# Optimization experiments

Hardware: AMD Instinct MI355X
Metric: run time of the kernel (lower is better)

Reference implementation:

```python
import jax, jax.numpy as jnp
import numpy as np

HEAD_DIM = 64
N_IT = 3
EPS = 1.0  # SinkhornDistance(1, max_iter=n_it)
SCALE = 1.0 / float(np.sqrt(HEAD_DIM))


def setup_inputs() -> dict:
    key = jax.random.key(0)
    kq, kk, kv = jax.random.split(key, 3)
    B, H, S, D = 2, 12, 1024, HEAD_DIM
    q = jax.random.normal(kq, (B, H, S, D), dtype=jnp.float32)
    k = jax.random.normal(kk, (B, H, S, D), dtype=jnp.float32)
    v = jax.random.normal(kv, (B, H, S, D), dtype=jnp.float32)
    attn_mask = jnp.zeros((1, 1, S, S), dtype=bool)  # False -> no position masked
    return {"q": q, "k": k, "v": v, "attn_mask": attn_mask}


def _sinkhorn(scores):
    # Log-domain Sinkhorn-Knopp (sinkformers-style). Cost C = -scores,
    # uniform marginals mu = nu = 1/S, u/v initialized to zero.
    C = -scores                                   # [N, S, S]
    n = C.shape[-2]
    m = C.shape[-1]
    log_mu = -jnp.log(jnp.asarray(n, C.dtype))    # log(1/n)
    log_nu = -jnp.log(jnp.asarray(m, C.dtype))    # log(1/m)

    def M(u, v):
        # modified cost matrix: (-C + u_i + v_j) / eps
        return (-C + u[..., :, None] + v[..., None, :]) / EPS

    def body(carry, _):
        u, v = carry
        u = EPS * (log_mu - jax.scipy.special.logsumexp(M(u, v), axis=-1)) + u
        v = EPS * (log_nu - jax.scipy.special.logsumexp(M(u, v), axis=-2)) + v
        return (u, v), None

    u0 = jnp.zeros(C.shape[:-1], C.dtype)
    v0 = jnp.zeros(C.shape[:-2] + (m,), C.dtype)
    (u, v), _ = jax.lax.scan(body, (u0, v0), None, length=N_IT)
    return jnp.exp(M(u, v))                       # transport plan pi, rows/cols ~ 1/S


def reference(q, k, v, attn_mask):
    B, H, S, D = q.shape
    scores = jnp.einsum('bhqd,bhkd->bhqk', q, k) * SCALE
    scores = jnp.where(attn_mask, jnp.asarray(-1e9, scores.dtype), scores)
    pi = _sinkhorn(scores.reshape(B * H, S, S))
    # pi rows sum to ~1/S; multiply by S so rows sum to ~1 (as in the torch code)
    attn_weights = (pi * S).reshape(B, H, S, S)
    output = jnp.einsum('bhqk,bhkd->bhqd', attn_weights, v)
    return output, attn_weights
```

## Files before the change

### kernel.cpp

```cpp
#include <hip/hip_runtime.h>
#include <hip/hip_fp16.h>
#include <cstddef>
#include <cstdint>


#define NH 24
#define SEQ 1024
#define HD 64
#define NHS (NH * SEQ)

typedef _Float16 f16x8 __attribute__((ext_vector_type(8)));
typedef float f32x4 __attribute__((ext_vector_type(4)));

__global__ __launch_bounds__(256) void k_prep(const float* __restrict__ q,
                                              const float* __restrict__ kin,
                                              const float* __restrict__ v,
                                              __half* __restrict__ q16,
                                              __half* __restrict__ k16,
                                              __half* __restrict__ vt16,
                                              float* __restrict__ zvec) {
  const int b = blockIdx.x;
  const int z = b / 768;
  const int bb = b - z * 768;
  const int t = threadIdx.x;
  if (z < 2) {
    const float* src = z ? kin : q;
    __half* dst = z ? k16 : q16;
    size_t u = ((size_t)bb * 256 + t) * 8;
    const float4* s4 = (const float4*)(src + u);
    float4 a = s4[0], c = s4[1];
    f16x8 h;
    h[0] = (_Float16)a.x; h[1] = (_Float16)a.y; h[2] = (_Float16)a.z; h[3] = (_Float16)a.w;
    h[4] = (_Float16)c.x; h[5] = (_Float16)c.y; h[6] = (_Float16)c.z; h[7] = (_Float16)c.w;
    *(f16x8*)(dst + u) = h;
    if (z == 0) {
      int gid = bb * 256 + t;
      if (gid < 6 * NHS) zvec[gid] = 0.f;
    }
  } else {
    __shared__ float ld[64][33];
    const int h = bb >> 5, s0 = (bb & 31) << 5;
    const float* Vh = v + (size_t)h * SEQ * HD;
#pragma unroll
    for (int it = 0; it < 2; ++it) {
      int f = t + (it << 8);
      int r = f >> 4, c4 = (f & 15) << 2;
      float4 vv = *(const float4*)(Vh + (size_t)(s0 + r) * HD + c4);
      ld[c4 + 0][r] = vv.x; ld[c4 + 1][r] = vv.y;
      ld[c4 + 2][r] = vv.z; ld[c4 + 3][r] = vv.w;
    }
    __syncthreads();
    int d = t >> 2, sg = (t & 3) << 3;
    f16x8 h8;
#pragma unroll
    for (int i = 0; i < 8; ++i) h8[i] = (_Float16)ld[d][sg + i];
    *(f16x8*)(vt16 + (size_t)h * HD * SEQ + (size_t)d * SEQ + s0 + sg) = h8;
  }
}

template <int MODE>
__global__ __launch_bounds__(256) void k_sweep(const __half* __restrict__ q16,
                                               const __half* __restrict__ k16,
                                               const float* __restrict__ vecPrev,
                                               float* __restrict__ vecOut) {
  __shared__ __align__(16) __half ks[128][72];
  __shared__ float ws_[128];
  const int bid = blockIdx.x;
  const int swz = (bid & 7) * 192 + (bid >> 3);
  const int h = swz >> 6;
  const int row0 = ((swz >> 3) & 7) << 7;
  const int col0 = (swz & 7) << 7;
  const int t = threadIdx.x;
  const int w = t >> 6, lane = t & 63;
  const int ln = lane & 15, ko = lane >> 4;
  const int rb = (w & 1) << 6, cb = (w >> 1) << 6;
  const __half* qh = q16 + ((size_t)h << 16);
  const __half* kh = k16 + ((size_t)h << 16);

#pragma unroll
  for (int it = 0; it < 4; ++it) {
    int f = t + (it << 8);
    int row = f >> 3, c8 = (f & 7) << 3;
    *(f16x8*)&ks[row][c8] = *(const f16x8*)(kh + (size_t)(col0 + row) * HD + c8);
  }
  if (MODE == 1 && t < 128) ws_[t] = (1.0f / 1024.0f) / vecPrev[h * SEQ + col0 + t];
  if (MODE == 2 && t < 128) ws_[t] = (1.0f / 1024.0f) / vecPrev[h * SEQ + row0 + t];
  f16x8 af[4][2];
#pragma unroll
  for (int m = 0; m < 4; ++m)
#pragma unroll
    for (int kk = 0; kk < 2; ++kk)
      af[m][kk] = *(const f16x8*)(qh + (size_t)(row0 + rb + m * 16 + ln) * HD + kk * 32 + ko * 8);
  __syncthreads();

  f32x4 acc[4][4] = {};
#pragma unroll
  for (int kk = 0; kk < 2; ++kk) {
    f16x8 bf[4];
#pragma unroll
    for (int n = 0; n < 4; ++n)
      bf[n] = *(const f16x8*)&ks[cb + n * 16 + ln][kk * 32 + ko * 8];
#pragma unroll
    for (int m = 0; m < 4; ++m)
#pragma unroll
      for (int n = 0; n < 4; ++n)
        acc[m][n] = __builtin_amdgcn_mfma_f32_16x16x32_f16(af[m][kk], bf[n], acc[m][n], 0, 0, 0);
  }

#pragma unroll
  for (int m = 0; m < 4; ++m)
#pragma unroll
    for (int n = 0; n < 4; ++n)
#pragma unroll
      for (int r = 0; r < 4; ++r)
        acc[m][n][r] = __expf(acc[m][n][r] * 0.125f);

  if (MODE == 2) {
    float* cs = vecOut + h * SEQ;
#pragma unroll
    for (int n = 0; n < 4; ++n) {
      float s = 0.f;
#pragma unroll
      for (int m = 0; m < 4; ++m)
#pragma unroll
        for (int r = 0; r < 4; ++r)
          s += acc[m][n][r] * ws_[rb + m * 16 + (ko << 2) + r];
      s += __shfl_xor(s, 16);
      s += __shfl_xor(s, 32);
      if (lane < 16) atomicAdd(&cs[col0 + cb + n * 16 + ln], s);
    }
  } else {
    float* rd = vecOut + h * SEQ;
#pragma unroll
    for (int m = 0; m < 4; ++m)
#pragma unroll
      for (int r = 0; r < 4; ++r) {
        float s;
        if (MODE == 1) {
          s = acc[m][0][r] * ws_[cb + ln] + acc[m][1][r] * ws_[cb + 16 + ln]
            + acc[m][2][r] * ws_[cb + 32 + ln] + acc[m][3][r] * ws_[cb + 48 + ln];
        } else {
          s = acc[m][0][r] + acc[m][1][r] + acc[m][2][r] + acc[m][3][r];
        }
        s += __shfl_xor(s, 1, 16); s += __shfl_xor(s, 2, 16);
        s += __shfl_xor(s, 4, 16); s += __shfl_xor(s, 8, 16);
        if (ln == 0) atomicAdd(&rd[row0 + rb + m * 16 + (ko << 2) + r], s);
      }
  }
}

__global__ __launch_bounds__(256) void k_final(const __half* __restrict__ q16,
                                               const __half* __restrict__ k16,
                                               const __half* __restrict__ vt16,
                                               const float* __restrict__ rd2,
                                               const float* __restrict__ cs2,
                                               float* __restrict__ attn,
                                               float* __restrict__ out) {
  __shared__ __align__(16) __half ps16[2][16][136];
  __shared__ float binv[1024];
  __shared__ float a_s[16];
  const int bid = blockIdx.x;
  const int swz = (bid & 7) * 192 + (bid >> 3);
  const int h = swz >> 6;
  const int rblk = swz & 63;
  const int t = threadIdx.x;
  const int w = t >> 6, lane = t & 63, ln = lane & 15, ko = lane >> 4;

#pragma unroll
  for (int i = 0; i < 4; ++i) {
    int idx = t + (i << 8);
    binv[idx] = 1.0f / cs2[h * SEQ + idx];
  }
  if (t < 16) a_s[t] = (1.0f / 1024.0f) / rd2[h * SEQ + rblk * 16 + t];

  const __half* qh = q16 + ((size_t)h << 16);
  const __half* kh = k16 + ((size_t)h << 16);
  const __half* vth = vt16 + ((size_t)h << 16);
  f16x8 aq[2];
#pragma unroll
  for (int kk = 0; kk < 2; ++kk)
    aq[kk] = *(const f16x8*)(qh + (size_t)(rblk * 16 + ln) * HD + kk * 32 + ko * 8);

  const int cw = w << 5;
  const int dw = w << 4;

  f16x8 kf00, kf01, kf10, kf11;
  kf00 = *(const f16x8*)(kh + (size_t)(cw + ln) * HD + ko * 8);
  kf01 = *(const f16x8*)(kh + (size_t)(cw + 16 + ln) * HD + ko * 8);
  kf10 = *(const f16x8*)(kh + (size_t)(cw + ln) * HD + 32 + ko * 8);
  kf11 = *(const f16x8*)(kh + (size_t)(cw + 16 + ln) * HD + 32 + ko * 8);
  f16x8 vf0, vf1, vf2, vf3;
  {
    const __half* vb = vth + (size_t)(dw + ln) * SEQ;
    vf0 = *(const f16x8*)(vb + ko * 8);
    vf1 = *(const f16x8*)(vb + 32 + ko * 8);
    vf2 = *(const f16x8*)(vb + 64 + ko * 8);
    vf3 = *(const f16x8*)(vb + 96 + ko * 8);
  }
  f32x4 sacc0 = {}, sacc1 = {};
  sacc0 = __builtin_amdgcn_mfma_f32_16x16x32_f16(aq[0], kf00, sacc0, 0, 0, 0);
  sacc1 = __builtin_amdgcn_mfma_f32_16x16x32_f16(aq[0], kf01, sacc1, 0, 0, 0);
  sacc0 = __builtin_amdgcn_mfma_f32_16x16x32_f16(aq[1], kf10, sacc0, 0, 0, 0);
  sacc1 = __builtin_amdgcn_mfma_f32_16x16x32_f16(aq[1], kf11, sacc1, 0, 0, 0);
  f32x4 acc_o = {};
  __syncthreads();

  for (int c = 0; c < 8; ++c) {
    const int j0 = c << 7;
    const int buf = c & 1;
    f16x8 kn00, kn01, kn10, kn11, vn0, vn1, vn2, vn3;
    if (c < 7) {
      const __half* kb = kh + (size_t)(j0 + 128) * HD;
      kn00 = *(const f16x8*)(kb + (size_t)(cw + ln) * HD + ko * 8);
      kn01 = *(const f16x8*)(kb + (size_t)(cw + 16 + ln) * HD + ko * 8);
      kn10 = *(const f16x8*)(kb + (size_t)(cw + ln) * HD + 32 + ko * 8);
      kn11 = *(const f16x8*)(kb + (size_t)(cw + 16 + ln) * HD + 32 + ko * 8);
      const __half* vb = vth + (size_t)(dw + ln) * SEQ + j0 + 128;
      vn0 = *(const f16x8*)(vb + ko * 8);
      vn1 = *(const f16x8*)(vb + 32 + ko * 8);
      vn2 = *(const f16x8*)(vb + 64 + ko * 8);
      vn3 = *(const f16x8*)(vb + 96 + ko * 8);
    }
#pragma unroll
    for (int r = 0; r < 4; ++r) {
      int row = (ko << 2) + r;
      int c0 = cw + ln, c1 = cw + 16 + ln;
      ps16[buf][row][c0] = __float2half(__expf(sacc0[r] * 0.125f) * a_s[row] * binv[j0 + c0]);
      ps16[buf][row][c1] = __float2half(__expf(sacc1[r] * 0.125f) * a_s[row] * binv[j0 + c1]);
    }
    __syncthreads();
    {
      int arow = t >> 4, cg = (t & 15) << 3;
      f16x8 hv = *(const f16x8*)&ps16[buf][arow][cg];
      f32x4 o0, o1;
#pragma unroll
      for (int i = 0; i < 4; ++i) { o0[i] = (float)hv[i]; o1[i] = (float)hv[4 + i]; }
      float* ap = attn + (size_t)(h * SEQ + rblk * 16 + arow) * SEQ + j0 + cg;
      *(f32x4*)ap = o0;
      *(f32x4*)(ap + 4) = o1;
    }
    {
      f16x8 pa;
      pa = *(const f16x8*)&ps16[buf][ln][ko * 8];
      acc_o = __builtin_amdgcn_mfma_f32_16x16x32_f16(pa, vf0, acc_o, 0, 0, 0);
      pa = *(const f16x8*)&ps16[buf][ln][32 + ko * 8];
      acc_o = __builtin_amdgcn_mfma_f32_16x16x32_f16(pa, vf1, acc_o, 0, 0, 0);
      pa = *(const f16x8*)&ps16[buf][ln][64 + ko * 8];
      acc_o = __builtin_amdgcn_mfma_f32_16x16x32_f16(pa, vf2, acc_o, 0, 0, 0);
      pa = *(const f16x8*)&ps16[buf][ln][96 + ko * 8];
      acc_o = __builtin_amdgcn_mfma_f32_16x16x32_f16(pa, vf3, acc_o, 0, 0, 0);
    }
    if (c < 7) {
      sacc0 = (f32x4){};
      sacc1 = (f32x4){};
      sacc0 = __builtin_amdgcn_mfma_f32_16x16x32_f16(aq[0], kn00, sacc0, 0, 0, 0);
      sacc1 = __builtin_amdgcn_mfma_f32_16x16x32_f16(aq[0], kn01, sacc1, 0, 0, 0);
      sacc0 = __builtin_amdgcn_mfma_f32_16x16x32_f16(aq[1], kn10, sacc0, 0, 0, 0);
      sacc1 = __builtin_amdgcn_mfma_f32_16x16x32_f16(aq[1], kn11, sacc1, 0, 0, 0);
      vf0 = vn0; vf1 = vn1; vf2 = vn2; vf3 = vn3;
    }
  }

#pragma unroll
  for (int r = 0; r < 4; ++r)
    out[(size_t)(h * SEQ + rblk * 16 + (ko << 2) + r) * HD + dw + ln] = acc_o[r];
}

extern "C" void kernel_launch(void* const* d_in, const int* in_sizes, int n_in,
                              void* d_out, int out_size, void* d_ws, size_t ws_size,
                              hipStream_t stream) {
  const float* q = (const float*)d_in[0];
  const float* k = (const float*)d_in[1];
  const float* v = (const float*)d_in[2];
  (void)in_sizes; (void)n_in; (void)out_size; (void)ws_size;

  float* out = (float*)d_out;
  float* attn = out + (size_t)NH * SEQ * HD;

  float* wsf = (float*)d_ws;
  float* rd0 = wsf;
  float* cs0 = wsf + 1 * NHS;
  float* rd1 = wsf + 2 * NHS;
  float* cs1 = wsf + 3 * NHS;
  float* rd2 = wsf + 4 * NHS;
  float* cs2 = wsf + 5 * NHS;
  __half* q16 = (__half*)(wsf + 6 * NHS);
  __half* k16 = q16 + (size_t)NH * SEQ * HD;
  __half* vt16 = k16 + (size_t)NH * SEQ * HD;

  k_prep<<<2304, 256, 0, stream>>>(q, k, v, q16, k16, vt16, wsf);
  k_sweep<0><<<1536, 256, 0, stream>>>(q16, k16, rd0, rd0);
  k_sweep<2><<<1536, 256, 0, stream>>>(q16, k16, rd0, cs0);
  k_sweep<1><<<1536, 256, 0, stream>>>(q16, k16, cs0, rd1);
  k_sweep<2><<<1536, 256, 0, stream>>>(q16, k16, rd1, cs1);
  k_sweep<1><<<1536, 256, 0, stream>>>(q16, k16, cs1, rd2);
  k_sweep<2><<<1536, 256, 0, stream>>>(q16, k16, rd2, cs2);
  k_final<<<1536, 256, 0, stream>>>(q16, k16, vt16, rd2, cs2, attn, out);
}
```

Measured before the change: 136.4 us.

## Fuse Sinkhorn sweeps into persistent kernel with register-resident scores and grid barriers

Replaces the six separate sweep launches with one persistent kernel of 768 blocks, each owning two 128x128 score tiles. It computes exp(QK^T) once, keeps the tiles in registers, and runs the row and column normalization passes with software grid barriers between them. This removes five recomputations of the QK^T matmul and exp, along with the extra kernel launches. The cost is higher register pressure, and the kernel depends on all 768 blocks being co-resident for the spin barrier, otherwise it can deadlock.

```diff
diff --git a/kernel.cpp b/kernel.cpp
--- a/kernel.cpp
+++ b/kernel.cpp
@@ -8,9 +8,23 @@
 #define SEQ 1024
 #define HD 64
 #define NHS (NH * SEQ)
+#define GRID_SINK 768
 
 typedef _Float16 f16x8 __attribute__((ext_vector_type(8)));
 typedef float f32x4 __attribute__((ext_vector_type(4)));
+
+__device__ __forceinline__ float aload(float* p) {
+  return __hip_atomic_load(p, __ATOMIC_RELAXED, __HIP_MEMORY_SCOPE_AGENT);
+}
+__device__ __forceinline__ void gbar(unsigned* cnt, unsigned target) {
+  __syncthreads();
+  if (threadIdx.x == 0) {
+    __hip_atomic_fetch_add(cnt, 1u, __ATOMIC_ACQ_REL, __HIP_MEMORY_SCOPE_AGENT);
+    while (__hip_atomic_load(cnt, __ATOMIC_ACQUIRE, __HIP_MEMORY_SCOPE_AGENT) < target)
+      __builtin_amdgcn_s_sleep(2);
+  }
+  __syncthreads();
+}
 
 __global__ __launch_bounds__(256) void k_prep(const float* __restrict__ q,
                                               const float* __restrict__ kin,
@@ -36,6 +50,7 @@
     if (z == 0) {
       int gid = bb * 256 + t;
       if (gid < 6 * NHS) zvec[gid] = 0.f;
+      else if (gid == 6 * NHS) *(unsigned*)(zvec + 6 * NHS) = 0u;
     }
   } else {
     __shared__ float ld[64][33];
@@ -58,95 +73,140 @@
   }
 }
 
-template <int MODE>
-__global__ __launch_bounds__(256) void k_sweep(const __half* __restrict__ q16,
-                                               const __half* __restrict__ k16,
-                                               const float* __restrict__ vecPrev,
-                                               float* __restrict__ vecOut) {
-  __shared__ __align__(16) __half ks[128][72];
-  __shared__ float ws_[128];
+__global__ __launch_bounds__(256, 4) void k_sink(const __half* __restrict__ q16,
+                                                 const __half* __restrict__ k16,
+                                                 float* __restrict__ vec,
+                                                 unsigned* __restrict__ cnt) {
+  __shared__ __align__(16) __half ks[2][128][72];
+  __shared__ float ws_[2][128];
   const int bid = blockIdx.x;
-  const int swz = (bid & 7) * 192 + (bid >> 3);
-  const int h = swz >> 6;
-  const int row0 = ((swz >> 3) & 7) << 7;
-  const int col0 = (swz & 7) << 7;
   const int t = threadIdx.x;
   const int w = t >> 6, lane = t & 63;
   const int ln = lane & 15, ko = lane >> 4;
   const int rb = (w & 1) << 6, cb = (w >> 1) << 6;
-  const __half* qh = q16 + ((size_t)h << 16);
-  const __half* kh = k16 + ((size_t)h << 16);
-
-#pragma unroll
-  for (int it = 0; it < 4; ++it) {
-    int f = t + (it << 8);
-    int row = f >> 3, c8 = (f & 7) << 3;
-    *(f16x8*)&ks[row][c8] = *(const f16x8*)(kh + (size_t)(col0 + row) * HD + c8);
-  }
-  if (MODE == 1 && t < 128) ws_[t] = (1.0f / 1024.0f) / vecPrev[h * SEQ + col0 + t];
-  if (MODE == 2 && t < 128) ws_[t] = (1.0f / 1024.0f) / vecPrev[h * SEQ + row0 + t];
-  f16x8 af[4][2];
-#pragma unroll
-  for (int m = 0; m < 4; ++m)
-#pragma unroll
-    for (int kk = 0; kk < 2; ++kk)
-      af[m][kk] = *(const f16x8*)(qh + (size_t)(row0 + rb + m * 16 + ln) * HD + kk * 32 + ko * 8);
+
+  int hh[2], r0[2], c0[2];
+#pragma unroll
+  for (int u = 0; u < 2; ++u) {
+    int b2 = bid + u * GRID_SINK;
+    int swz = (b2 & 7) * 192 + (b2 >> 3);
+    hh[u] = swz >> 6;
+    r0[u] = ((swz >> 3) & 7) << 7;
+    c0[u] = (swz & 7) << 7;
+  }
+
+#pragma unroll
+  for (int u = 0; u < 2; ++u) {
+    const __half* kh = k16 + ((size_t)hh[u] << 16);
+#pragma unroll
+    for (int it = 0; it < 4; ++it) {
+      int f = t + (it << 8);
+      int row = f >> 3, c8 = (f & 7) << 3;
+      *(f16x8*)&ks[u][row][c8] = *(const f16x8*)(kh + (size_t)(c0[u] + row) * HD + c8);
+    }
+  }
   __syncthreads();
 
-  f32x4 acc[4][4] = {};
-#pragma unroll
-  for (int kk = 0; kk < 2; ++kk) {
-    f16x8 bf[4];
-#pragma unroll
-    for (int n = 0; n < 4; ++n)
-      bf[n] = *(const f16x8*)&ks[cb + n * 16 + ln][kk * 32 + ko * 8];
+  f32x4 p[2][4][4] = {};
+#pragma unroll
+  for (int u = 0; u < 2; ++u) {
+    const __half* qh = q16 + ((size_t)hh[u] << 16);
+    f16x8 af[4][2];
 #pragma unroll
     for (int m = 0; m < 4; ++m)
 #pragma unroll
+      for (int kk = 0; kk < 2; ++kk)
+        af[m][kk] = *(const f16x8*)(qh + (size_t)(r0[u] + rb + m * 16 + ln) * HD + kk * 32 + ko * 8);
+#pragma unroll
+    for (int kk = 0; kk < 2; ++kk) {
+      f16x8 bf[4];
+#pragma unroll
       for (int n = 0; n < 4; ++n)
-        acc[m][n] = __builtin_amdgcn_mfma_f32_16x16x32_f16(af[m][kk], bf[n], acc[m][n], 0, 0, 0);
-  }
-
-#pragma unroll
-  for (int m = 0; m < 4; ++m)
-#pragma unroll
-    for (int n = 0; n < 4; ++n)
-#pragma unroll
-      for (int r = 0; r < 4; ++r)
-        acc[m][n][r] = __expf(acc[m][n][r] * 0.125f);
-
-  if (MODE == 2) {
-    float* cs = vecOut + h * SEQ;
-#pragma unroll
-    for (int n = 0; n < 4; ++n) {
-      float s = 0.f;
+        bf[n] = *(const f16x8*)&ks[u][cb + n * 16 + ln][kk * 32 + ko * 8];
 #pragma unroll
       for (int m = 0; m < 4; ++m)
 #pragma unroll
+        for (int n = 0; n < 4; ++n)
+          p[u][m][n] = __builtin_amdgcn_mfma_f32_16x16x32_f16(af[m][kk], bf[n], p[u][m][n], 0, 0, 0);
+    }
+  }
+#pragma unroll
+  for (int u = 0; u < 2; ++u)
+#pragma unroll
+    for (int m = 0; m < 4; ++m)
+#pragma unroll
+      for (int n = 0; n < 4; ++n)
+#pragma unroll
         for (int r = 0; r < 4; ++r)
-          s += acc[m][n][r] * ws_[rb + m * 16 + (ko << 2) + r];
-      s += __shfl_xor(s, 16);
-      s += __shfl_xor(s, 32);
-      if (lane < 16) atomicAdd(&cs[col0 + cb + n * 16 + ln], s);
-    }
-  } else {
-    float* rd = vecOut + h * SEQ;
+          p[u][m][n][r] = __expf(p[u][m][n][r] * 0.125f);
+
+  float* v0 = vec;
+  float* v1 = vec + 1 * NHS;
+  float* v2 = vec + 2 * NHS;
+  float* v3 = vec + 3 * NHS;
+  float* v4 = vec + 4 * NHS;
+  float* v5 = vec + 5 * NHS;
+
+  auto colpass = [&](float* src_rd, float* dst_cs) {
+    if (t < 128) {
+      ws_[0][t] = (1.0f / 1024.0f) / aload(&src_rd[hh[0] * SEQ + r0[0] + t]);
+      ws_[1][t] = (1.0f / 1024.0f) / aload(&src_rd[hh[1] * SEQ + r0[1] + t]);
+    }
+    __syncthreads();
+#pragma unroll
+    for (int u = 0; u < 2; ++u)
+#pragma unroll
+      for (int n = 0; n < 4; ++n) {
+        float s = 0.f;
+#pragma unroll
+        for (int m = 0; m < 4; ++m)
+#pragma unroll
+          for (int r = 0; r < 4; ++r)
+            s += p[u][m][n][r] * ws_[u][rb + m * 16 + (ko << 2) + r];
+        s += __shfl_xor(s, 16);
+        s += __shfl_xor(s, 32);
+        if (lane < 16) atomicAdd(&dst_cs[hh[u] * SEQ + c0[u] + cb + n * 16 + ln], s);
+      }
+  };
+  auto rowpass = [&](float* src_cs, float* dst_rd) {
+    if (t < 128) {
+      ws_[0][t] = (1.0f / 1024.0f) / aload(&src_cs[hh[0] * SEQ + c0[0] + t]);
+      ws_[1][t] = (1.0f / 1024.0f) / aload(&src_cs[hh[1] * SEQ + c0[1] + t]);
+    }
+    __syncthreads();
+#pragma unroll
+    for (int u = 0; u < 2; ++u)
+#pragma unroll
+      for (int m = 0; m < 4; ++m)
+#pragma unroll
+        for (int r = 0; r < 4; ++r) {
+          float s = p[u][m][0][r] * ws_[u][cb + ln]
+                  + p[u][m][1][r] * ws_[u][cb + 16 + ln]
+                  + p[u][m][2][r] * ws_[u][cb + 32 + ln]
+                  + p[u][m][3][r] * ws_[u][cb + 48 + ln];
+          s += __shfl_xor(s, 1, 16); s += __shfl_xor(s, 2, 16);
+          s += __shfl_xor(s, 4, 16); s += __shfl_xor(s, 8, 16);
+          if (ln == 0) atomicAdd(&dst_rd[hh[u] * SEQ + r0[u] + rb + m * 16 + (ko << 2) + r], s);
+        }
+  };
+
+#pragma unroll
+  for (int u = 0; u < 2; ++u)
 #pragma unroll
     for (int m = 0; m < 4; ++m)
 #pragma unroll
       for (int r = 0; r < 4; ++r) {
-        float s;
-        if (MODE == 1) {
-          s = acc[m][0][r] * ws_[cb + ln] + acc[m][1][r] * ws_[cb + 16 + ln]
-            + acc[m][2][r] * ws_[cb + 32 + ln] + acc[m][3][r] * ws_[cb + 48 + ln];
-        } else {
-          s = acc[m][0][r] + acc[m][1][r] + acc[m][2][r] + acc[m][3][r];
-        }
+        float s = p[u][m][0][r] + p[u][m][1][r] + p[u][m][2][r] + p[u][m][3][r];
         s += __shfl_xor(s, 1, 16); s += __shfl_xor(s, 2, 16);
         s += __shfl_xor(s, 4, 16); s += __shfl_xor(s, 8, 16);
-        if (ln == 0) atomicAdd(&rd[row0 + rb + m * 16 + (ko << 2) + r], s);
+        if (ln == 0) atomicAdd(&v0[hh[u] * SEQ + r0[u] + rb + m * 16 + (ko << 2) + r], s);
       }
-  }
+  gbar(cnt, 1 * GRID_SINK);
+  colpass(v0, v1);  gbar(cnt, 2 * GRID_SINK);
+  rowpass(v1, v2);  gbar(cnt, 3 * GRID_SINK);
+  colpass(v2, v3);  gbar(cnt, 4 * GRID_SINK);
+  rowpass(v3, v4);  gbar(cnt, 5 * GRID_SINK);
+  colpass(v4, v5);
 }
 
 __global__ __launch_bounds__(256) void k_final(const __half* __restrict__ q16,
@@ -224,9 +284,9 @@
 #pragma unroll
     for (int r = 0; r < 4; ++r) {
       int row = (ko << 2) + r;
-      int c0 = cw + ln, c1 = cw + 16 + ln;
-      ps16[buf][row][c0] = __float2half(__expf(sacc0[r] * 0.125f) * a_s[row] * binv[j0 + c0]);
-      ps16[buf][row][c1] = __float2half(__expf(sacc1[r] * 0.125f) * a_s[row] * binv[j0 + c1]);
+      int cA = cw + ln, cB = cw + 16 + ln;
+      ps16[buf][row][cA] = __float2half(__expf(sacc0[r] * 0.125f) * a_s[row] * binv[j0 + cA]);
+      ps16[buf][row][cB] = __float2half(__expf(sacc1[r] * 0.125f) * a_s[row] * binv[j0 + cB]);
     }
     __syncthreads();
     {
@@ -278,22 +338,13 @@
   float* attn = out + (size_t)NH * SEQ * HD;
 
   float* wsf = (float*)d_ws;
-  float* rd0 = wsf;
-  float* cs0 = wsf + 1 * NHS;
-  float* rd1 = wsf + 2 * NHS;
-  float* cs1 = wsf + 3 * NHS;
-  float* rd2 = wsf + 4 * NHS;
-  float* cs2 = wsf + 5 * NHS;
-  __half* q16 = (__half*)(wsf + 6 * NHS);
+  float* vec = wsf;
+  unsigned* cnt = (unsigned*)(wsf + 6 * NHS);
+  __half* q16 = (__half*)(wsf + 6 * NHS + 64);
   __half* k16 = q16 + (size_t)NH * SEQ * HD;
   __half* vt16 = k16 + (size_t)NH * SEQ * HD;
 
   k_prep<<<2304, 256, 0, stream>>>(q, k, v, q16, k16, vt16, wsf);
-  k_sweep<0><<<1536, 256, 0, stream>>>(q16, k16, rd0, rd0);
-  k_sweep<2><<<1536, 256, 0, stream>>>(q16, k16, rd0, cs0);
-  k_sweep<1><<<1536, 256, 0, stream>>>(q16, k16, cs0, rd1);
-  k_sweep<2><<<1536, 256, 0, stream>>>(q16, k16, rd1, cs1);
-  k_sweep<1><<<1536, 256, 0, stream>>>(q16, k16, cs1, rd2);
-  k_sweep<2><<<1536, 256, 0, stream>>>(q16, k16, rd2, cs2);
-  k_final<<<1536, 256, 0, stream>>>(q16, k16, vt16, rd2, cs2, attn, out);
-}
+  k_sink<<<GRID_SINK, 256, 0, stream>>>(q16, k16, vec, cnt);
+  k_final<<<1536, 256, 0, stream>>>(q16, k16, vt16, vec + 4 * NHS, vec + 5 * NHS, attn, out);
+}
```

Measured after the change: 394.6 us. +189.3%, slower.
